# Kernel tuning notes

Measured on AMD Instinct MI355X. Metric: run time of the kernel, lower is better.

Reference implementation:

```python
import jax, jax.numpy as jnp
import numpy as np

N_NODES = 100000
N_EDGES = 1600000
N_GRAPHS = 512


def gcn_conv(x, src, dst, W, b, n_nodes):
    """PyG GCNConv: add self-loops, symmetric norm, linear, scatter-add, bias."""
    h = x @ W.T                                   # [N, out]
    ones = jnp.ones(src.shape[0], dtype=x.dtype)
    deg = jax.ops.segment_sum(ones, dst, num_segments=n_nodes)   # in-degree incl. self-loops
    dinv = jnp.where(deg > 0, jax.lax.rsqrt(deg), 0.0)
    norm = dinv[src] * dinv[dst]                  # [E+N]
    msg = h[src] * norm[:, None]                  # gather + scale
    out = jax.ops.segment_sum(msg, dst, num_segments=n_nodes)
    return out + b


def setup_inputs() -> dict:
    key = jax.random.key(0)
    ks = jax.random.split(key, 8)
    x = jax.random.normal(ks[0], (N_NODES, 2), dtype=jnp.float32)
    edge_index = jax.random.randint(ks[1], (2, N_EDGES), 0, N_NODES, dtype=jnp.int64)
    batch = jnp.sort(jax.random.randint(ks[2], (N_NODES,), 0, N_GRAPHS, dtype=jnp.int64))
    def glorot(k, shape):
        lim = jnp.sqrt(6.0 / (shape[0] + shape[1])).astype(jnp.float32)
        return jax.random.uniform(k, shape, jnp.float32, -lim, lim)
    return {
        "x": x, "edge_index": edge_index, "batch": batch,
        "W1": glorot(ks[3], (32, 2)),  "b1": jnp.zeros(32, jnp.float32),
        "W2": glorot(ks[4], (64, 32)), "b2": jnp.zeros(64, jnp.float32),
        "W3": glorot(ks[5], (32, 64)), "b3": jnp.zeros(32, jnp.float32),
        "Wfc": glorot(ks[6], (1, 32)), "bfc": jnp.zeros(1, jnp.float32),
    }


def reference(x, edge_index, batch, W1, b1, W2, b2, W3, b3, Wfc, bfc):
    n = x.shape[0]
    loop = jnp.arange(n, dtype=edge_index.dtype)
    src = jnp.concatenate([edge_index[0], loop])  # self-loops appended once
    dst = jnp.concatenate([edge_index[1], loop])

    h = jax.nn.relu(gcn_conv(x, src, dst, W1, b1, n))   # dropout = identity (eval)
    h = jax.nn.relu(gcn_conv(h, src, dst, W2, b2, n))
    h = jax.nn.relu(gcn_conv(h, src, dst, W3, b3, n))

    # global_mean_pool over graph ids
    sums = jax.ops.segment_sum(h, batch, num_segments=N_GRAPHS)
    cnts = jax.ops.segment_sum(jnp.ones((n,), h.dtype), batch, num_segments=N_GRAPHS)
    pooled = sums / jnp.maximum(cnts, 1.0)[:, None]     # [G, 32]
    return pooled @ Wfc.T + bfc                         # [G, 1]
```

## Files before the change

kernel.cpp:

```cpp
#include <hip/hip_runtime.h>
#include <hip/hip_fp16.h>


static constexpr int TPB = 256;
static constexpr int NB1 = 256;
static constexpr int NB_SCAN = 256;
static constexpr int P2CAP = 6144;

__global__ void p1_hist_gptr_kernel(const int* __restrict__ dst, int* __restrict__ hist,
                                    int E, int chunk, int shift, int B,
                                    const int* __restrict__ batch, int* __restrict__ gstart,
                                    int n, int G) {
  int b = blockIdx.x, t = threadIdx.x;
  if (b >= NB1) {
    int i = (b - NB1) * TPB + t;
    if (i >= n) return;
    int bb = batch[i];
    int bp = (i == 0) ? -1 : batch[i - 1];
    for (int g = bp + 1; g <= bb; ++g) gstart[g] = i;
    if (i == n - 1)
      for (int g = bb + 1; g <= G; ++g) gstart[g] = n;
    return;
  }
  __shared__ int h[1024];
  for (int i = t; i < B; i += TPB) h[i] = 0;
  __syncthreads();
  int lo = b * chunk, hi = min(lo + chunk, E);
  for (int e = lo + t; e < hi; e += TPB) atomicAdd(&h[dst[e] >> shift], 1);
  __syncthreads();
  for (int i = t; i < B; i += TPB) hist[i * NB1 + b] = h[i];
}

__global__ void scan_partial_kernel(const int* __restrict__ a, int* __restrict__ bsum,
                                    int n, int seg) {
  int b = blockIdx.x, t = threadIdx.x;
  int lo = b * seg, hi = min(lo + seg, n);
  int acc = 0;
  for (int i = lo + t; i < hi; i += TPB) acc += a[i];
  __shared__ int red[TPB];
  red[t] = acc;
  __syncthreads();
  for (int st = TPB / 2; st > 0; st >>= 1) {
    if (t < st) red[t] += red[t + st];
    __syncthreads();
  }
  if (t == 0) bsum[b] = red[0];
}

__global__ void scan_emit_kernel(int* __restrict__ a, const int* __restrict__ bsum,
                                 int n, int seg) {
  int b = blockIdx.x, t = threadIdx.x;
  int lo = b * seg, hi = min(lo + seg, n);
  __shared__ int cs[TPB];
  __shared__ int s_run;
  cs[t] = (t < b) ? bsum[t] : 0;
  __syncthreads();
  for (int st = TPB / 2; st > 0; st >>= 1) {
    if (t < st) cs[t] += cs[t + st];
    __syncthreads();
  }
  if (t == 0) s_run = cs[0];
  __syncthreads();
  for (int base = lo; base < hi; base += TPB) {
    int i = base + t;
    int v = (i < hi) ? a[i] : 0;
    cs[t] = v;
    __syncthreads();
    for (int off = 1; off < TPB; off <<= 1) {
      int u = (t >= off) ? cs[t - off] : 0;
      __syncthreads();
      cs[t] += u;
      __syncthreads();
    }
    if (i < hi) a[i] = s_run + cs[t] - v;
    __syncthreads();
    if (t == 0) s_run += cs[TPB - 1];
    __syncthreads();
  }
}

__global__ void p1_scatter_kernel(const int* __restrict__ src, const int* __restrict__ dst,
                                  const int* __restrict__ hist, unsigned int* __restrict__ epk,
                                  int E, int chunk, int shift, int srcbits, int B) {
  __shared__ int cur[1024];
  int b = blockIdx.x, t = threadIdx.x;
  for (int i = t; i < B; i += TPB) cur[i] = hist[i * NB1 + b];
  __syncthreads();
  int lo = b * chunk, hi = min(lo + chunk, E);
  int span1 = (1 << shift) - 1;
  for (int e = lo + t; e < hi; e += TPB) {
    int d = dst[e];
    int pos = atomicAdd(&cur[d >> shift], 1);
    epk[pos] = ((unsigned int)(d & span1) << srcbits) | (unsigned int)src[e];
  }
}

__global__ __launch_bounds__(TPB) void p2_sort_kernel(
    const unsigned int* __restrict__ epk, const int* __restrict__ hist,
    const float2* __restrict__ x2,
    int* __restrict__ rowptr, float* __restrict__ dinv, float2* __restrict__ u0,
    int* __restrict__ esrc, int N, int E, int shift, int srcbits, int B) {
  int bkt = blockIdx.x, t = threadIdx.x;
  int span = 1 << shift;
  unsigned int smask = (1u << srcbits) - 1u;
  int nb = bkt << shift;
  int bstart = hist[bkt * NB1];
  int bend = (bkt + 1 < B) ? hist[(bkt + 1) * NB1] : E;
  int bsize = bend - bstart;
  __shared__ int cnt[256];
  __shared__ int ex[256];
  __shared__ int ldata[P2CAP];
  __shared__ int lsrc[P2CAP];
  bool stage = (bsize <= P2CAP);
  if (t < span) cnt[t] = 0;
  __syncthreads();
  if (stage) {
    for (int i = t; i < bsize; i += TPB) ldata[i] = (int)epk[bstart + i];
    __syncthreads();
    for (int i = t; i < bsize; i += TPB)
      atomicAdd(&cnt[((unsigned int)ldata[i]) >> srcbits], 1);
  } else {
    for (int e = bstart + t; e < bend; e += TPB) atomicAdd(&cnt[epk[e] >> srcbits], 1);
  }
  __syncthreads();
  int v = (t < span) ? cnt[t] : 0;
  ex[t] = v;
  __syncthreads();
  for (int off = 1; off < 256; off <<= 1) {
    int u = (t >= off) ? ex[t - off] : 0;
    __syncthreads();
    ex[t] += u;
    __syncthreads();
  }
  int excl = ex[t] - v;
  int node = nb + t;
  if (t < span && node < N) {
    rowptr[node] = bstart + excl;
    float dv = rsqrtf((float)v + 1.0f);
    dinv[node] = dv;
    float2 xv = x2[node];
    u0[node] = make_float2(xv.x * dv, xv.y * dv);
  }
  if (bkt == 0 && t == 0) rowptr[N] = E;
  __syncthreads();
  if (t < span) cnt[t] = stage ? excl : bstart + excl;
  __syncthreads();
  if (stage) {
    for (int i = t; i < bsize; i += TPB) {
      unsigned int p = (unsigned int)ldata[i];
      int pos = atomicAdd(&cnt[p >> srcbits], 1);
      lsrc[pos] = (int)(p & smask);
    }
    __syncthreads();
    for (int i = t; i < bsize; i += TPB) esrc[bstart + i] = lsrc[i];
  } else {
    for (int e = bstart + t; e < bend; e += TPB) {
      unsigned int p = epk[e];
      int pos = atomicAdd(&cnt[p >> srcbits], 1);
      esrc[pos] = (int)(p & smask);
    }
  }
}

__global__ void layer1_kernel(const float2* __restrict__ u0, const int* __restrict__ rowptr,
                              const int* __restrict__ esrc, const float* __restrict__ W1,
                              const float* __restrict__ b1, const float* __restrict__ dinv,
                              __half* __restrict__ u1_16, int n) {
  int tid = blockIdx.x * blockDim.x + threadIdx.x;
  int i = tid >> 2, split = tid & 3;
  if (i >= n) return;
  float ax = 0.f, ay = 0.f;
  if (split == 0) {
    float2 s = u0[i];
    ax = s.x; ay = s.y;
  }
  int r0 = rowptr[i], r1 = rowptr[i + 1];
  int e = r0 + split;
  if (e < r1) {
    int snext = esrc[e];
    for (e += 4; e < r1; e += 4) {
      int scur = snext;
      snext = esrc[e];
      float2 v = u0[scur];
      ax += v.x; ay += v.y;
    }
    float2 v = u0[snext];
    ax += v.x; ay += v.y;
  }
  ax += __shfl_xor(ax, 1, 64); ay += __shfl_xor(ay, 1, 64);
  ax += __shfl_xor(ax, 2, 64); ay += __shfl_xor(ay, 2, 64);
  float di = dinv[i];
  int f0 = split * 8;
  union { float4 f4[1]; __half h[8]; } oh;
#pragma unroll
  for (int k = 0; k < 8; ++k) {
    int f = f0 + k;
    float hv = fmaxf(di * (W1[f * 2 + 0] * ax + W1[f * 2 + 1] * ay) + b1[f], 0.f);
    oh.h[k] = __float2half(di * hv);
  }
  *(float4*)&u1_16[(size_t)i * 32 + f0] = oh.f4[0];
}

template <bool EPI>
__global__ void gather32_kernel(const float4* __restrict__ a16,
                                const int* __restrict__ rowptr, const int* __restrict__ esrc,
                                const float* __restrict__ dinv, const float* __restrict__ b,
                                float4* __restrict__ out16, int n) {
  int tid = blockIdx.x * blockDim.x + threadIdx.x;
  int i = tid >> 4;
  int sub = tid & 15;
  int split = sub >> 2, q = sub & 3;
  if (i >= n) return;
  float acc[8] = {0.f, 0.f, 0.f, 0.f, 0.f, 0.f, 0.f, 0.f};
  auto addrow = [&](int s) {
    union { float4 f4; __half2 h2[4]; } u;
    u.f4 = a16[(size_t)s * 4 + q];
    float2 a0 = __half22float2(u.h2[0]);
    float2 a1 = __half22float2(u.h2[1]);
    float2 a2 = __half22float2(u.h2[2]);
    float2 a3 = __half22float2(u.h2[3]);
    acc[0] += a0.x; acc[1] += a0.y; acc[2] += a1.x; acc[3] += a1.y;
    acc[4] += a2.x; acc[5] += a2.y; acc[6] += a3.x; acc[7] += a3.y;
  };
  if (split == 0) addrow(i);
  int r0 = rowptr[i], r1 = rowptr[i + 1];
  int e = r0 + split;
  if (e < r1) {
    int snext = esrc[e];
    for (e += 4; e < r1; e += 4) {
      int scur = snext;
      snext = esrc[e];
      addrow(scur);
    }
    addrow(snext);
  }
#pragma unroll
  for (int k = 0; k < 8; ++k) acc[k] += __shfl_xor(acc[k], 4, 64);
#pragma unroll
  for (int k = 0; k < 8; ++k) acc[k] += __shfl_xor(acc[k], 8, 64);
  if (split != 0) return;
  if (EPI) {
    float di = dinv[i];
    const float4 bv0 = ((const float4*)b)[2 * q];
    const float4 bv1 = ((const float4*)b)[2 * q + 1];
    acc[0] = fmaxf(di * acc[0] + bv0.x, 0.f);
    acc[1] = fmaxf(di * acc[1] + bv0.y, 0.f);
    acc[2] = fmaxf(di * acc[2] + bv0.z, 0.f);
    acc[3] = fmaxf(di * acc[3] + bv0.w, 0.f);
    acc[4] = fmaxf(di * acc[4] + bv1.x, 0.f);
    acc[5] = fmaxf(di * acc[5] + bv1.y, 0.f);
    acc[6] = fmaxf(di * acc[6] + bv1.z, 0.f);
    acc[7] = fmaxf(di * acc[7] + bv1.w, 0.f);
  }
  union { float4 f4; __half2 h2[4]; } o;
  o.h2[0] = __floats2half2_rn(acc[0], acc[1]);
  o.h2[1] = __floats2half2_rn(acc[2], acc[3]);
  o.h2[2] = __floats2half2_rn(acc[4], acc[5]);
  o.h2[3] = __floats2half2_rn(acc[6], acc[7]);
  out16[(size_t)i * 4 + q] = o.f4;
}

__global__ __launch_bounds__(TPB) void t2t3_kernel(
    const float4* __restrict__ U1h, const float* __restrict__ W2, const float* __restrict__ b2,
    const float* __restrict__ W3, const float* __restrict__ dinv,
    __half* __restrict__ g3_16, int n) {
  constexpr int SN = 136;
  __shared__ float U1l[32 * SN];
  __shared__ float h2l[64 * SN];
  __shared__ float W2l[32 * 68];
  __shared__ float W3l[64 * 36];
  __shared__ float dil[128];
  int t = threadIdx.x;
  int base = blockIdx.x * 128;
  for (int idx = t; idx < 2048; idx += TPB) {
    int k = idx >> 5, j = idx & 31;
    W2l[j * 68 + k] = W2[idx];
  }
  for (int idx = t; idx < 2048; idx += TPB) {
    int k = idx >> 6, j = idx & 63;
    W3l[j * 36 + k] = W3[idx];
  }
  if (t < 128) dil[t] = (base + t < n) ? dinv[base + t] : 0.f;
  for (int it = 0; it < 2; ++it) {
    int idx = it * 256 + t;
    int nl = idx >> 2, j0 = (idx & 3) * 8;
    int node = base + nl;
    union { float4 f4; __half2 h2[4]; } u;
    u.f4 = (node < n) ? U1h[(size_t)node * 4 + (idx & 3)]
                      : make_float4(0.f, 0.f, 0.f, 0.f);
#pragma unroll
    for (int k = 0; k < 4; ++k) {
      float2 p = __half22float2(u.h2[k]);
      U1l[(j0 + 2 * k + 0) * SN + nl] = p.x;
      U1l[(j0 + 2 * k + 1) * SN + nl] = p.y;
    }
  }
  __syncthreads();
  {
    int a = t & 15, bb = t >> 4;
    int n0 = a * 8, k0 = bb * 4;
    float acc[4][8];
#pragma unroll
    for (int kk = 0; kk < 4; ++kk)
#pragma unroll
      for (int nn = 0; nn < 8; ++nn) acc[kk][nn] = 0.f;
#pragma unroll 8
    for (int j = 0; j < 32; ++j) {
      float4 ua = *(const float4*)&U1l[j * SN + n0];
      float4 ub = *(const float4*)&U1l[j * SN + n0 + 4];
      float4 w = *(const float4*)&W2l[j * 68 + k0];
      float un[8] = {ua.x, ua.y, ua.z, ua.w, ub.x, ub.y, ub.z, ub.w};
      float wk[4] = {w.x, w.y, w.z, w.w};
#pragma unroll
      for (int kk = 0; kk < 4; ++kk)
#pragma unroll
        for (int nn = 0; nn < 8; ++nn) acc[kk][nn] += un[nn] * wk[kk];
    }
    float4 bv = ((const float4*)b2)[bb];
    float bk[4] = {bv.x, bv.y, bv.z, bv.w};
#pragma unroll
    for (int kk = 0; kk < 4; ++kk) {
      float o[8];
#pragma unroll
      for (int nn = 0; nn < 8; ++nn)
        o[nn] = fmaxf(dil[n0 + nn] * acc[kk][nn] + bk[kk], 0.f);
      *(float4*)&h2l[(k0 + kk) * SN + n0] = make_float4(o[0], o[1], o[2], o[3]);
      *(float4*)&h2l[(k0 + kk) * SN + n0 + 4] = make_float4(o[4], o[5], o[6], o[7]);
    }
  }
  __syncthreads();
  {
    int a = t & 15, bb = t >> 4;
    int n0 = a * 8, k0 = bb * 2;
    float acc[2][8];
#pragma unroll
    for (int kk = 0; kk < 2; ++kk)
#pragma unroll
      for (int nn = 0; nn < 8; ++nn) acc[kk][nn] = 0.f;
#pragma unroll 8
    for (int j = 0; j < 64; ++j) {
      float4 ua = *(const float4*)&h2l[j * SN + n0];
      float4 ub = *(const float4*)&h2l[j * SN + n0 + 4];
      float w0 = W3l[j * 36 + k0];
      float w1 = W3l[j * 36 + k0 + 1];
      float un[8] = {ua.x, ua.y, ua.z, ua.w, ub.x, ub.y, ub.z, ub.w};
#pragma unroll
      for (int nn = 0; nn < 8; ++nn) {
        acc[0][nn] += un[nn] * w0;
        acc[1][nn] += un[nn] * w1;
      }
    }
#pragma unroll
    for (int nn = 0; nn < 8; ++nn) {
      int node = base + n0 + nn;
      if (node < n) {
        float di = dil[n0 + nn];
        __half2 hv = __floats2half2_rn(di * acc[0][nn], di * acc[1][nn]);
        *(__half2*)&g3_16[(size_t)node * 32 + k0] = hv;
      }
    }
  }
}

__global__ void poolfc_kernel(const __half* __restrict__ h3, const int* __restrict__ gstart,
                              const float* __restrict__ Wfc, const float* __restrict__ bfc,
                              float* __restrict__ out) {
  int gi = blockIdx.x;
  int s = gstart[gi], e = gstart[gi + 1];
  int t = threadIdx.x;
  int nl = t >> 5, f = t & 31;
  float acc = 0.f;
  for (int i = s + nl; i < e; i += 8) acc += __half2float(h3[(size_t)i * 32 + f]);
  __shared__ float red[256];
  red[t] = acc;
  __syncthreads();
  for (int st = 128; st >= 32; st >>= 1) {
    if (t < st) red[t] += red[t + st];
    __syncthreads();
  }
  if (t < 32) {
    float cnt = (float)(e - s);
    float v = (red[t] / fmaxf(cnt, 1.f)) * Wfc[t];
    for (int o = 16; o; o >>= 1) v += __shfl_down(v, o, 32);
    if (t == 0) out[gi] = v + bfc[0];
  }
}

extern "C" void kernel_launch(void* const* d_in, const int* in_sizes, int n_in,
                              void* d_out, int out_size, void* d_ws, size_t ws_size,
                              hipStream_t stream) {
  const float* x     = (const float*)d_in[0];
  const int*   ei    = (const int*)d_in[1];
  const int*   batch = (const int*)d_in[2];
  const float* W1    = (const float*)d_in[3];
  const float* b1    = (const float*)d_in[4];
  const float* W2    = (const float*)d_in[5];
  const float* b2    = (const float*)d_in[6];
  const float* W3    = (const float*)d_in[7];
  const float* b3    = (const float*)d_in[8];
  const float* Wfc   = (const float*)d_in[9];
  const float* bfc   = (const float*)d_in[10];
  float* out = (float*)d_out;

  const int N = in_sizes[0] / 2;
  const int E = in_sizes[1] / 2;
  const int G = out_size;
  const int* src = ei;
  const int* dst = ei + E;

  int shift = 8;
  while ((((N + (1 << shift) - 1) >> shift)) > 1024) ++shift;
  const int B = (N + (1 << shift) - 1) >> shift;
  const int srcbits = 32 - shift;
  const int chunkE = (E + NB1 - 1) / NB1;
  const int M = B * NB1;
  const int segM = (M + NB_SCAN - 1) / NB_SCAN;

  char* ws = (char*)d_ws;
  size_t off = 0;
  auto alloc = [&](size_t bytes) -> char* {
    char* p = ws + off;
    off += (bytes + 255) & ~(size_t)255;
    return p;
  };
  float*        dinv   = (float*)alloc((size_t)N * 4);
  int*          rowptr = (int*)alloc((size_t)(N + 1) * 4);
  int*          esrc   = (int*)alloc((size_t)E * 4);
  int*          gstart = (int*)alloc((size_t)(G + 1) * 4);
  int*          hist   = (int*)alloc((size_t)M * 4);
  int*          bsum   = (int*)alloc((size_t)NB_SCAN * 4);
  unsigned int* epk    = (unsigned int*)alloc((size_t)E * 4);
  float2*       u0     = (float2*)alloc((size_t)N * 8);
  __half*       u1_16  = (__half*)alloc((size_t)N * 32 * 2);
  __half*       U1h    = (__half*)alloc((size_t)N * 32 * 2);
  __half*       g3_16  = (__half*)alloc((size_t)N * 32 * 2);
  __half*       hA16   = (__half*)alloc((size_t)N * 32 * 2);

  const int gptrBlocks = (N + TPB - 1) / TPB;
  p1_hist_gptr_kernel<<<NB1 + gptrBlocks, TPB, 0, stream>>>(dst, hist, E, chunkE, shift, B,
                                                            batch, gstart, N, G);
  scan_partial_kernel<<<NB_SCAN, TPB, 0, stream>>>(hist, bsum, M, segM);
  scan_emit_kernel<<<NB_SCAN, TPB, 0, stream>>>(hist, bsum, M, segM);
  p1_scatter_kernel<<<NB1, TPB, 0, stream>>>(src, dst, hist, epk, E, chunkE, shift, srcbits, B);
  p2_sort_kernel<<<B, TPB, 0, stream>>>(epk, hist, (const float2*)x, rowptr, dinv, u0, esrc,
                                        N, E, shift, srcbits, B);

  layer1_kernel<<<((size_t)N * 4 + TPB - 1) / TPB, TPB, 0, stream>>>(
      u0, rowptr, esrc, W1, b1, dinv, u1_16, N);

  gather32_kernel<false><<<((size_t)N * 16 + TPB - 1) / TPB, TPB, 0, stream>>>(
      (const float4*)u1_16, rowptr, esrc, dinv, b2, (float4*)U1h, N);
  t2t3_kernel<<<(N + 127) / 128, TPB, 0, stream>>>(
      (const float4*)U1h, W2, b2, W3, dinv, g3_16, N);

  gather32_kernel<true><<<((size_t)N * 16 + TPB - 1) / TPB, TPB, 0, stream>>>(
      (const float4*)g3_16, rowptr, esrc, dinv, b3, (float4*)hA16, N);

  poolfc_kernel<<<G, 256, 0, stream>>>(hA16, gstart, Wfc, bfc, out);
}
```

Measured before the change: 220.0 us.

## Fuse layer-2 gather with both dense transforms, unroll edge loops by two

```diff
diff --git a/kernel.cpp b/kernel.cpp
--- a/kernel.cpp
+++ b/kernel.cpp
@@ -176,15 +176,16 @@
   }
   int r0 = rowptr[i], r1 = rowptr[i + 1];
   int e = r0 + split;
+  while (e + 4 < r1) {
+    int s0 = esrc[e], s1 = esrc[e + 4];
+    float2 v0 = u0[s0];
+    float2 v1 = u0[s1];
+    ax += v0.x + v1.x;
+    ay += v0.y + v1.y;
+    e += 8;
+  }
   if (e < r1) {
-    int snext = esrc[e];
-    for (e += 4; e < r1; e += 4) {
-      int scur = snext;
-      snext = esrc[e];
-      float2 v = u0[scur];
-      ax += v.x; ay += v.y;
-    }
-    float2 v = u0[snext];
+    float2 v = u0[esrc[e]];
     ax += v.x; ay += v.y;
   }
   ax += __shfl_xor(ax, 1, 64); ay += __shfl_xor(ay, 1, 64);
@@ -201,20 +202,113 @@
   *(float4*)&u1_16[(size_t)i * 32 + f0] = oh.f4[0];
 }
 
-template <bool EPI>
-__global__ void gather32_kernel(const float4* __restrict__ a16,
-                                const int* __restrict__ rowptr, const int* __restrict__ esrc,
-                                const float* __restrict__ dinv, const float* __restrict__ b,
-                                float4* __restrict__ out16, int n) {
+__global__ __launch_bounds__(TPB) void gather_t2t3_kernel(
+    const float4* __restrict__ a16, const int* __restrict__ rowptr,
+    const int* __restrict__ esrc, const float* __restrict__ dinv,
+    const float* __restrict__ W2, const float* __restrict__ b2,
+    const float* __restrict__ W3, __half* __restrict__ g3_16, int n) {
+  __shared__ float U1l[16 * 33];
+  __shared__ float h2l[16 * 68];
+  __shared__ float W2l[32 * 68];
+  __shared__ float W3l[64 * 36];
+  __shared__ float dil[16];
+  int t = threadIdx.x;
+  int base = blockIdx.x * 16;
+  for (int idx = t; idx < 2048; idx += TPB) {
+    int k = idx >> 5, j = idx & 31;
+    W2l[j * 68 + k] = W2[idx];
+  }
+  for (int idx = t; idx < 2048; idx += TPB) {
+    int k = idx >> 6, j = idx & 63;
+    W3l[j * 36 + k] = W3[idx];
+  }
+  if (t < 16) dil[t] = (base + t < n) ? dinv[base + t] : 0.f;
+
+  int i = base + (t >> 4);
+  int sub = t & 15, split = sub >> 2, q = sub & 3;
+  float acc[8] = {0.f, 0.f, 0.f, 0.f, 0.f, 0.f, 0.f, 0.f};
+  if (i < n) {
+    auto addf4 = [&](float4 f) {
+      union { float4 f4; __half2 h2[4]; } u;
+      u.f4 = f;
+      float2 a0 = __half22float2(u.h2[0]);
+      float2 a1 = __half22float2(u.h2[1]);
+      float2 a2 = __half22float2(u.h2[2]);
+      float2 a3 = __half22float2(u.h2[3]);
+      acc[0] += a0.x; acc[1] += a0.y; acc[2] += a1.x; acc[3] += a1.y;
+      acc[4] += a2.x; acc[5] += a2.y; acc[6] += a3.x; acc[7] += a3.y;
+    };
+    if (split == 0) addf4(a16[(size_t)i * 4 + q]);
+    int r0 = rowptr[i], r1 = rowptr[i + 1];
+    int e = r0 + split;
+    while (e + 4 < r1) {
+      int s0 = esrc[e], s1 = esrc[e + 4];
+      float4 f0 = a16[(size_t)s0 * 4 + q];
+      float4 f1 = a16[(size_t)s1 * 4 + q];
+      addf4(f0);
+      addf4(f1);
+      e += 8;
+    }
+    if (e < r1) addf4(a16[(size_t)esrc[e] * 4 + q]);
+#pragma unroll
+    for (int k = 0; k < 8; ++k) acc[k] += __shfl_xor(acc[k], 4, 64);
+#pragma unroll
+    for (int k = 0; k < 8; ++k) acc[k] += __shfl_xor(acc[k], 8, 64);
+    if (split == 0) {
+      int nl = t >> 4;
+#pragma unroll
+      for (int k = 0; k < 8; ++k) U1l[nl * 33 + q * 8 + k] = acc[k];
+    }
+  }
+  __syncthreads();
+
+  {
+    int nl = t >> 4, k0 = (t & 15) * 4;
+    float a0 = 0.f, a1 = 0.f, a2 = 0.f, a3 = 0.f;
+#pragma unroll 8
+    for (int j = 0; j < 32; ++j) {
+      float u = U1l[nl * 33 + j];
+      float4 w = *(const float4*)&W2l[j * 68 + k0];
+      a0 += u * w.x; a1 += u * w.y; a2 += u * w.z; a3 += u * w.w;
+    }
+    float di = dil[nl];
+    float4 bv = ((const float4*)b2)[t & 15];
+    *(float4*)&h2l[nl * 68 + k0] =
+        make_float4(fmaxf(di * a0 + bv.x, 0.f), fmaxf(di * a1 + bv.y, 0.f),
+                    fmaxf(di * a2 + bv.z, 0.f), fmaxf(di * a3 + bv.w, 0.f));
+  }
+  __syncthreads();
+
+  {
+    int nl = t >> 4, k0 = (t & 15) * 2;
+    float a0 = 0.f, a1 = 0.f;
+#pragma unroll 8
+    for (int j = 0; j < 64; ++j) {
+      float u = h2l[nl * 68 + j];
+      a0 += u * W3l[j * 36 + k0];
+      a1 += u * W3l[j * 36 + k0 + 1];
+    }
+    int node = base + nl;
+    if (node < n) {
+      float di = dil[nl];
+      *(__half2*)&g3_16[(size_t)node * 32 + k0] = __floats2half2_rn(di * a0, di * a1);
+    }
+  }
+}
+
+__global__ void gather32epi_kernel(const float4* __restrict__ a16,
+                                   const int* __restrict__ rowptr, const int* __restrict__ esrc,
+                                   const float* __restrict__ dinv, const float* __restrict__ b,
+                                   float4* __restrict__ out16, int n) {
   int tid = blockIdx.x * blockDim.x + threadIdx.x;
   int i = tid >> 4;
   int sub = tid & 15;
   int split = sub >> 2, q = sub & 3;
   if (i >= n) return;
   float acc[8] = {0.f, 0.f, 0.f, 0.f, 0.f, 0.f, 0.f, 0.f};
-  auto addrow = [&](int s) {
+  auto addf4 = [&](float4 f) {
     union { float4 f4; __half2 h2[4]; } u;
-    u.f4 = a16[(size_t)s * 4 + q];
+    u.f4 = f;
     float2 a0 = __half22float2(u.h2[0]);
     float2 a1 = __half22float2(u.h2[1]);
     float2 a2 = __half22float2(u.h2[2]);
@@ -222,36 +316,34 @@
     acc[0] += a0.x; acc[1] += a0.y; acc[2] += a1.x; acc[3] += a1.y;
     acc[4] += a2.x; acc[5] += a2.y; acc[6] += a3.x; acc[7] += a3.y;
   };
-  if (split == 0) addrow(i);
+  if (split == 0) addf4(a16[(size_t)i * 4 + q]);
   int r0 = rowptr[i], r1 = rowptr[i + 1];
   int e = r0 + split;
-  if (e < r1) {
-    int snext = esrc[e];
-    for (e += 4; e < r1; e += 4) {
-      int scur = snext;
-      snext = esrc[e];
-      addrow(scur);
-    }
-    addrow(snext);
-  }
+  while (e + 4 < r1) {
+    int s0 = esrc[e], s1 = esrc[e + 4];
+    float4 f0 = a16[(size_t)s0 * 4 + q];
+    float4 f1 = a16[(size_t)s1 * 4 + q];
+    addf4(f0);
+    addf4(f1);
+    e += 8;
+  }
+  if (e < r1) addf4(a16[(size_t)esrc[e] * 4 + q]);
 #pragma unroll
   for (int k = 0; k < 8; ++k) acc[k] += __shfl_xor(acc[k], 4, 64);
 #pragma unroll
   for (int k = 0; k < 8; ++k) acc[k] += __shfl_xor(acc[k], 8, 64);
   if (split != 0) return;
-  if (EPI) {
-    float di = dinv[i];
-    const float4 bv0 = ((const float4*)b)[2 * q];
-    const float4 bv1 = ((const float4*)b)[2 * q + 1];
-    acc[0] = fmaxf(di * acc[0] + bv0.x, 0.f);
-    acc[1] = fmaxf(di * acc[1] + bv0.y, 0.f);
-    acc[2] = fmaxf(di * acc[2] + bv0.z, 0.f);
-    acc[3] = fmaxf(di * acc[3] + bv0.w, 0.f);
-    acc[4] = fmaxf(di * acc[4] + bv1.x, 0.f);
-    acc[5] = fmaxf(di * acc[5] + bv1.y, 0.f);
-    acc[6] = fmaxf(di * acc[6] + bv1.z, 0.f);
-    acc[7] = fmaxf(di * acc[7] + bv1.w, 0.f);
-  }
+  float di = dinv[i];
+  const float4 bv0 = ((const float4*)b)[2 * q];
+  const float4 bv1 = ((const float4*)b)[2 * q + 1];
+  acc[0] = fmaxf(di * acc[0] + bv0.x, 0.f);
+  acc[1] = fmaxf(di * acc[1] + bv0.y, 0.f);
+  acc[2] = fmaxf(di * acc[2] + bv0.z, 0.f);
+  acc[3] = fmaxf(di * acc[3] + bv0.w, 0.f);
+  acc[4] = fmaxf(di * acc[4] + bv1.x, 0.f);
+  acc[5] = fmaxf(di * acc[5] + bv1.y, 0.f);
+  acc[6] = fmaxf(di * acc[6] + bv1.z, 0.f);
+  acc[7] = fmaxf(di * acc[7] + bv1.w, 0.f);
   union { float4 f4; __half2 h2[4]; } o;
   o.h2[0] = __floats2half2_rn(acc[0], acc[1]);
   o.h2[1] = __floats2half2_rn(acc[2], acc[3]);
@@ -260,128 +352,29 @@
   out16[(size_t)i * 4 + q] = o.f4;
 }
 
-__global__ __launch_bounds__(TPB) void t2t3_kernel(
-    const float4* __restrict__ U1h, const float* __restrict__ W2, const float* __restrict__ b2,
-    const float* __restrict__ W3, const float* __restrict__ dinv,
-    __half* __restrict__ g3_16, int n) {
-  constexpr int SN = 136;
-  __shared__ float U1l[32 * SN];
-  __shared__ float h2l[64 * SN];
-  __shared__ float W2l[32 * 68];
-  __shared__ float W3l[64 * 36];
-  __shared__ float dil[128];
-  int t = threadIdx.x;
-  int base = blockIdx.x * 128;
-  for (int idx = t; idx < 2048; idx += TPB) {
-    int k = idx >> 5, j = idx & 31;
-    W2l[j * 68 + k] = W2[idx];
-  }
-  for (int idx = t; idx < 2048; idx += TPB) {
-    int k = idx >> 6, j = idx & 63;
-    W3l[j * 36 + k] = W3[idx];
-  }
-  if (t < 128) dil[t] = (base + t < n) ? dinv[base + t] : 0.f;
-  for (int it = 0; it < 2; ++it) {
-    int idx = it * 256 + t;
-    int nl = idx >> 2, j0 = (idx & 3) * 8;
-    int node = base + nl;
-    union { float4 f4; __half2 h2[4]; } u;
-    u.f4 = (node < n) ? U1h[(size_t)node * 4 + (idx & 3)]
-                      : make_float4(0.f, 0.f, 0.f, 0.f);
-#pragma unroll
-    for (int k = 0; k < 4; ++k) {
-      float2 p = __half22float2(u.h2[k]);
-      U1l[(j0 + 2 * k + 0) * SN + nl] = p.x;
-      U1l[(j0 + 2 * k + 1) * SN + nl] = p.y;
-    }
-  }
-  __syncthreads();
-  {
-    int a = t & 15, bb = t >> 4;
-    int n0 = a * 8, k0 = bb * 4;
-    float acc[4][8];
-#pragma unroll
-    for (int kk = 0; kk < 4; ++kk)
-#pragma unroll
-      for (int nn = 0; nn < 8; ++nn) acc[kk][nn] = 0.f;
-#pragma unroll 8
-    for (int j = 0; j < 32; ++j) {
-      float4 ua = *(const float4*)&U1l[j * SN + n0];
-      float4 ub = *(const float4*)&U1l[j * SN + n0 + 4];
-      float4 w = *(const float4*)&W2l[j * 68 + k0];
-      float un[8] = {ua.x, ua.y, ua.z, ua.w, ub.x, ub.y, ub.z, ub.w};
-      float wk[4] = {w.x, w.y, w.z, w.w};
-#pragma unroll
-      for (int kk = 0; kk < 4; ++kk)
-#pragma unroll
-        for (int nn = 0; nn < 8; ++nn) acc[kk][nn] += un[nn] * wk[kk];
-    }
-    float4 bv = ((const float4*)b2)[bb];
-    float bk[4] = {bv.x, bv.y, bv.z, bv.w};
-#pragma unroll
-    for (int kk = 0; kk < 4; ++kk) {
-      float o[8];
-#pragma unroll
-      for (int nn = 0; nn < 8; ++nn)
-        o[nn] = fmaxf(dil[n0 + nn] * acc[kk][nn] + bk[kk], 0.f);
-      *(float4*)&h2l[(k0 + kk) * SN + n0] = make_float4(o[0], o[1], o[2], o[3]);
-      *(float4*)&h2l[(k0 + kk) * SN + n0 + 4] = make_float4(o[4], o[5], o[6], o[7]);
-    }
-  }
-  __syncthreads();
-  {
-    int a = t & 15, bb = t >> 4;
-    int n0 = a * 8, k0 = bb * 2;
-    float acc[2][8];
-#pragma unroll
-    for (int kk = 0; kk < 2; ++kk)
-#pragma unroll
-      for (int nn = 0; nn < 8; ++nn) acc[kk][nn] = 0.f;
-#pragma unroll 8
-    for (int j = 0; j < 64; ++j) {
-      float4 ua = *(const float4*)&h2l[j * SN + n0];
-      float4 ub = *(const float4*)&h2l[j * SN + n0 + 4];
-      float w0 = W3l[j * 36 + k0];
-      float w1 = W3l[j * 36 + k0 + 1];
-      float un[8] = {ua.x, ua.y, ua.z, ua.w, ub.x, ub.y, ub.z, ub.w};
-#pragma unroll
-      for (int nn = 0; nn < 8; ++nn) {
-        acc[0][nn] += un[nn] * w0;
-        acc[1][nn] += un[nn] * w1;
-      }
-    }
-#pragma unroll
-    for (int nn = 0; nn < 8; ++nn) {
-      int node = base + n0 + nn;
-      if (node < n) {
-        float di = dil[n0 + nn];
-        __half2 hv = __floats2half2_rn(di * acc[0][nn], di * acc[1][nn]);
-        *(__half2*)&g3_16[(size_t)node * 32 + k0] = hv;
-      }
-    }
-  }
-}
-
-__global__ void poolfc_kernel(const __half* __restrict__ h3, const int* __restrict__ gstart,
+__global__ void poolfc_kernel(const __half2* __restrict__ h3, const int* __restrict__ gstart,
                               const float* __restrict__ Wfc, const float* __restrict__ bfc,
                               float* __restrict__ out) {
   int gi = blockIdx.x;
   int s = gstart[gi], e = gstart[gi + 1];
   int t = threadIdx.x;
-  int nl = t >> 5, f = t & 31;
-  float acc = 0.f;
-  for (int i = s + nl; i < e; i += 8) acc += __half2float(h3[(size_t)i * 32 + f]);
-  __shared__ float red[256];
-  red[t] = acc;
-  __syncthreads();
-  for (int st = 128; st >= 32; st >>= 1) {
-    if (t < st) red[t] += red[t + st];
-    __syncthreads();
-  }
-  if (t < 32) {
-    float cnt = (float)(e - s);
-    float v = (red[t] / fmaxf(cnt, 1.f)) * Wfc[t];
-    for (int o = 16; o; o >>= 1) v += __shfl_down(v, o, 32);
+  int nl = t >> 4, f2 = t & 15;
+  float ax = 0.f, ay = 0.f;
+  for (int i = s + nl; i < e; i += 16) {
+    float2 v = __half22float2(h3[(size_t)i * 16 + f2]);
+    ax += v.x; ay += v.y;
+  }
+  __shared__ float redx[256], redy[256];
+  redx[t] = ax; redy[t] = ay;
+  __syncthreads();
+  for (int st = 128; st >= 16; st >>= 1) {
+    if (t < st) { redx[t] += redx[t + st]; redy[t] += redy[t + st]; }
+    __syncthreads();
+  }
+  if (t < 16) {
+    float cnt = fmaxf((float)(e - s), 1.f);
+    float v = (redx[t] / cnt) * Wfc[2 * t] + (redy[t] / cnt) * Wfc[2 * t + 1];
+    for (int o = 8; o; o >>= 1) v += __shfl_down(v, o, 16);
     if (t == 0) out[gi] = v + bfc[0];
   }
 }
@@ -432,7 +425,6 @@
   unsigned int* epk    = (unsigned int*)alloc((size_t)E * 4);
   float2*       u0     = (float2*)alloc((size_t)N * 8);
   __half*       u1_16  = (__half*)alloc((size_t)N * 32 * 2);
-  __half*       U1h    = (__half*)alloc((size_t)N * 32 * 2);
   __half*       g3_16  = (__half*)alloc((size_t)N * 32 * 2);
   __half*       hA16   = (__half*)alloc((size_t)N * 32 * 2);
 
@@ -448,13 +440,11 @@
   layer1_kernel<<<((size_t)N * 4 + TPB - 1) / TPB, TPB, 0, stream>>>(
       u0, rowptr, esrc, W1, b1, dinv, u1_16, N);
 
-  gather32_kernel<false><<<((size_t)N * 16 + TPB - 1) / TPB, TPB, 0, stream>>>(
-      (const float4*)u1_16, rowptr, esrc, dinv, b2, (float4*)U1h, N);
-  t2t3_kernel<<<(N + 127) / 128, TPB, 0, stream>>>(
-      (const float4*)U1h, W2, b2, W3, dinv, g3_16, N);
-
-  gather32_kernel<true><<<((size_t)N * 16 + TPB - 1) / TPB, TPB, 0, stream>>>(
+  gather_t2t3_kernel<<<((size_t)N * 16 + TPB - 1) / TPB, TPB, 0, stream>>>(
+      (const float4*)u1_16, rowptr, esrc, dinv, W2, b2, W3, g3_16, N);
+
+  gather32epi_kernel<<<((size_t)N * 16 + TPB - 1) / TPB, TPB, 0, stream>>>(
       (const float4*)g3_16, rowptr, esrc, dinv, b3, (float4*)hA16, N);
 
-  poolfc_kernel<<<G, 256, 0, stream>>>(hA16, gstart, Wfc, bfc, out);
-}
+  poolfc_kernel<<<G, 256, 0, stream>>>((const __half2*)hA16, gstart, Wfc, bfc, out);
+}
```

Result: no change. 217.4 us (-1.2%).

## Replace per-node gather with block-level edge-parallel LDS atomic push aggregation

Applied to the files above, without the earlier changes.

```diff
diff --git a/kernel.cpp b/kernel.cpp
--- a/kernel.cpp
+++ b/kernel.cpp
@@ -102,7 +102,6 @@
     int* __restrict__ esrc, int N, int E, int shift, int srcbits, int B) {
   int bkt = blockIdx.x, t = threadIdx.x;
   int span = 1 << shift;
-  unsigned int smask = (1u << srcbits) - 1u;
   int nb = bkt << shift;
   int bstart = hist[bkt * NB1];
   int bend = (bkt + 1 < B) ? hist[(bkt + 1) * NB1] : E;
@@ -147,9 +146,9 @@
   __syncthreads();
   if (stage) {
     for (int i = t; i < bsize; i += TPB) {
-      unsigned int p = (unsigned int)ldata[i];
-      int pos = atomicAdd(&cnt[p >> srcbits], 1);
-      lsrc[pos] = (int)(p & smask);
+      int p = ldata[i];
+      int pos = atomicAdd(&cnt[((unsigned int)p) >> srcbits], 1);
+      lsrc[pos] = p;
     }
     __syncthreads();
     for (int i = t; i < bsize; i += TPB) esrc[bstart + i] = lsrc[i];
@@ -157,7 +156,7 @@
     for (int e = bstart + t; e < bend; e += TPB) {
       unsigned int p = epk[e];
       int pos = atomicAdd(&cnt[p >> srcbits], 1);
-      esrc[pos] = (int)(p & smask);
+      esrc[pos] = (int)p;
     }
   }
 }
@@ -165,10 +164,11 @@
 __global__ void layer1_kernel(const float2* __restrict__ u0, const int* __restrict__ rowptr,
                               const int* __restrict__ esrc, const float* __restrict__ W1,
                               const float* __restrict__ b1, const float* __restrict__ dinv,
-                              __half* __restrict__ u1_16, int n) {
+                              __half* __restrict__ u1_16, int n, int srcbits) {
   int tid = blockIdx.x * blockDim.x + threadIdx.x;
   int i = tid >> 2, split = tid & 3;
   if (i >= n) return;
+  unsigned int smask = (1u << srcbits) - 1u;
   float ax = 0.f, ay = 0.f;
   if (split == 0) {
     float2 s = u0[i];
@@ -176,15 +176,16 @@
   }
   int r0 = rowptr[i], r1 = rowptr[i + 1];
   int e = r0 + split;
+  while (e + 4 < r1) {
+    int s0 = esrc[e] & smask, s1 = esrc[e + 4] & smask;
+    float2 v0 = u0[s0];
+    float2 v1 = u0[s1];
+    ax += v0.x + v1.x;
+    ay += v0.y + v1.y;
+    e += 8;
+  }
   if (e < r1) {
-    int snext = esrc[e];
-    for (e += 4; e < r1; e += 4) {
-      int scur = snext;
-      snext = esrc[e];
-      float2 v = u0[scur];
-      ax += v.x; ay += v.y;
-    }
-    float2 v = u0[snext];
+    float2 v = u0[esrc[e] & smask];
     ax += v.x; ay += v.y;
   }
   ax += __shfl_xor(ax, 1, 64); ay += __shfl_xor(ay, 1, 64);
@@ -202,45 +203,61 @@
 }
 
 template <bool EPI>
-__global__ void gather32_kernel(const float4* __restrict__ a16,
-                                const int* __restrict__ rowptr, const int* __restrict__ esrc,
-                                const float* __restrict__ dinv, const float* __restrict__ b,
-                                float4* __restrict__ out16, int n) {
-  int tid = blockIdx.x * blockDim.x + threadIdx.x;
-  int i = tid >> 4;
-  int sub = tid & 15;
-  int split = sub >> 2, q = sub & 3;
-  if (i >= n) return;
-  float acc[8] = {0.f, 0.f, 0.f, 0.f, 0.f, 0.f, 0.f, 0.f};
-  auto addrow = [&](int s) {
+__global__ __launch_bounds__(TPB) void gpush_kernel(
+    const float4* __restrict__ a16, const int* __restrict__ rowptr,
+    const int* __restrict__ esrc, const float* __restrict__ dinv,
+    const float* __restrict__ b, float4* __restrict__ out16, int n, int srcbits) {
+  __shared__ float accum[64 * 33];
+  int t = threadIdx.x;
+  int base = blockIdx.x * 64;
+  unsigned int smask = (1u << srcbits) - 1u;
+  int nl = t >> 2, q = t & 3;
+  int node = base + nl;
+  {
     union { float4 f4; __half2 h2[4]; } u;
-    u.f4 = a16[(size_t)s * 4 + q];
-    float2 a0 = __half22float2(u.h2[0]);
-    float2 a1 = __half22float2(u.h2[1]);
-    float2 a2 = __half22float2(u.h2[2]);
-    float2 a3 = __half22float2(u.h2[3]);
-    acc[0] += a0.x; acc[1] += a0.y; acc[2] += a1.x; acc[3] += a1.y;
-    acc[4] += a2.x; acc[5] += a2.y; acc[6] += a3.x; acc[7] += a3.y;
-  };
-  if (split == 0) addrow(i);
-  int r0 = rowptr[i], r1 = rowptr[i + 1];
-  int e = r0 + split;
-  if (e < r1) {
-    int snext = esrc[e];
-    for (e += 4; e < r1; e += 4) {
-      int scur = snext;
-      snext = esrc[e];
-      addrow(scur);
-    }
-    addrow(snext);
-  }
-#pragma unroll
-  for (int k = 0; k < 8; ++k) acc[k] += __shfl_xor(acc[k], 4, 64);
-#pragma unroll
-  for (int k = 0; k < 8; ++k) acc[k] += __shfl_xor(acc[k], 8, 64);
-  if (split != 0) return;
+    u.f4 = (node < n) ? a16[(size_t)node * 4 + q] : make_float4(0.f, 0.f, 0.f, 0.f);
+    float* dstp = &accum[nl * 33 + q * 8];
+#pragma unroll
+    for (int k = 0; k < 4; ++k) {
+      float2 p = __half22float2(u.h2[k]);
+      dstp[2 * k + 0] = p.x;
+      dstp[2 * k + 1] = p.y;
+    }
+  }
+  __syncthreads();
+  int e0 = rowptr[base];
+  int e1 = rowptr[min(base + 64, n)];
+  int ne = e1 - e0;
+  int slot = t >> 2;
+  int nIter = (ne + 63) >> 6;
+  int my0 = slot * nIter;
+  for (int it = 0; it < nIter; ++it) {
+    int ei = my0 + it;
+    if (ei < ne) {
+      unsigned int p = (unsigned int)esrc[e0 + ei];
+      int src = (int)(p & smask);
+      int dl = (int)(p >> srcbits) & 63;
+      union { float4 f4; __half2 h2[4]; } u;
+      u.f4 = a16[(size_t)src * 4 + q];
+      float* ap = &accum[dl * 33 + q * 8];
+#pragma unroll
+      for (int k = 0; k < 4; ++k) {
+        float2 v = __half22float2(u.h2[k]);
+        atomicAdd(&ap[2 * k + 0], v.x);
+        atomicAdd(&ap[2 * k + 1], v.y);
+      }
+    }
+  }
+  __syncthreads();
+  if (node >= n) return;
+  float acc[8];
+  {
+    const float* sp = &accum[nl * 33 + q * 8];
+#pragma unroll
+    for (int k = 0; k < 8; ++k) acc[k] = sp[k];
+  }
   if (EPI) {
-    float di = dinv[i];
+    float di = dinv[node];
     const float4 bv0 = ((const float4*)b)[2 * q];
     const float4 bv1 = ((const float4*)b)[2 * q + 1];
     acc[0] = fmaxf(di * acc[0] + bv0.x, 0.f);
@@ -257,7 +274,7 @@
   o.h2[1] = __floats2half2_rn(acc[2], acc[3]);
   o.h2[2] = __floats2half2_rn(acc[4], acc[5]);
   o.h2[3] = __floats2half2_rn(acc[6], acc[7]);
-  out16[(size_t)i * 4 + q] = o.f4;
+  out16[(size_t)node * 4 + q] = o.f4;
 }
 
 __global__ __launch_bounds__(TPB) void t2t3_kernel(
@@ -362,26 +379,29 @@
   }
 }
 
-__global__ void poolfc_kernel(const __half* __restrict__ h3, const int* __restrict__ gstart,
+__global__ void poolfc_kernel(const __half2* __restrict__ h3, const int* __restrict__ gstart,
                               const float* __restrict__ Wfc, const float* __restrict__ bfc,
                               float* __restrict__ out) {
   int gi = blockIdx.x;
   int s = gstart[gi], e = gstart[gi + 1];
   int t = threadIdx.x;
-  int nl = t >> 5, f = t & 31;
-  float acc = 0.f;
-  for (int i = s + nl; i < e; i += 8) acc += __half2float(h3[(size_t)i * 32 + f]);
-  __shared__ float red[256];
-  red[t] = acc;
-  __syncthreads();
-  for (int st = 128; st >= 32; st >>= 1) {
-    if (t < st) red[t] += red[t + st];
-    __syncthreads();
-  }
-  if (t < 32) {
-    float cnt = (float)(e - s);
-    float v = (red[t] / fmaxf(cnt, 1.f)) * Wfc[t];
-    for (int o = 16; o; o >>= 1) v += __shfl_down(v, o, 32);
+  int nl = t >> 4, f2 = t & 15;
+  float ax = 0.f, ay = 0.f;
+  for (int i = s + nl; i < e; i += 16) {
+    float2 v = __half22float2(h3[(size_t)i * 16 + f2]);
+    ax += v.x; ay += v.y;
+  }
+  __shared__ float redx[256], redy[256];
+  redx[t] = ax; redy[t] = ay;
+  __syncthreads();
+  for (int st = 128; st >= 16; st >>= 1) {
+    if (t < st) { redx[t] += redx[t + st]; redy[t] += redy[t + st]; }
+    __syncthreads();
+  }
+  if (t < 16) {
+    float cnt = fmaxf((float)(e - s), 1.f);
+    float v = (redx[t] / cnt) * Wfc[2 * t] + (redy[t] / cnt) * Wfc[2 * t + 1];
+    for (int o = 8; o; o >>= 1) v += __shfl_down(v, o, 16);
     if (t == 0) out[gi] = v + bfc[0];
   }
 }
@@ -446,15 +466,16 @@
                                         N, E, shift, srcbits, B);
 
   layer1_kernel<<<((size_t)N * 4 + TPB - 1) / TPB, TPB, 0, stream>>>(
-      u0, rowptr, esrc, W1, b1, dinv, u1_16, N);
-
-  gather32_kernel<false><<<((size_t)N * 16 + TPB - 1) / TPB, TPB, 0, stream>>>(
-      (const float4*)u1_16, rowptr, esrc, dinv, b2, (float4*)U1h, N);
+      u0, rowptr, esrc, W1, b1, dinv, u1_16, N, srcbits);
+
+  const int gpushBlocks = (N + 63) / 64;
+  gpush_kernel<false><<<gpushBlocks, TPB, 0, stream>>>(
+      (const float4*)u1_16, rowptr, esrc, dinv, b2, (float4*)U1h, N, srcbits);
   t2t3_kernel<<<(N + 127) / 128, TPB, 0, stream>>>(
       (const float4*)U1h, W2, b2, W3, dinv, g3_16, N);
 
-  gather32_kernel<true><<<((size_t)N * 16 + TPB - 1) / TPB, TPB, 0, stream>>>(
-      (const float4*)g3_16, rowptr, esrc, dinv, b3, (float4*)hA16, N);
-
-  poolfc_kernel<<<G, 256, 0, stream>>>(hA16, gstart, Wfc, bfc, out);
-}
+  gpush_kernel<true><<<gpushBlocks, TPB, 0, stream>>>(
+      (const float4*)g3_16, rowptr, esrc, dinv, b3, (float4*)hA16, N, srcbits);
+
+  poolfc_kernel<<<G, 256, 0, stream>>>((const __half2*)hA16, gstart, Wfc, bfc, out);
+}
```

After: 770.6 us. 3.5x slower.

## Fuse mean-pool into last gather via atomic per-graph sums; unroll layer1 loop

Applied to the files above, without the earlier changes.

```diff
diff --git a/kernel.cpp b/kernel.cpp
--- a/kernel.cpp
+++ b/kernel.cpp
@@ -10,10 +10,11 @@
 __global__ void p1_hist_gptr_kernel(const int* __restrict__ dst, int* __restrict__ hist,
                                     int E, int chunk, int shift, int B,
                                     const int* __restrict__ batch, int* __restrict__ gstart,
-                                    int n, int G) {
+                                    float* __restrict__ gsum, int n, int G) {
   int b = blockIdx.x, t = threadIdx.x;
   if (b >= NB1) {
     int i = (b - NB1) * TPB + t;
+    if (i < G * 32) gsum[i] = 0.f;
     if (i >= n) return;
     int bb = batch[i];
     int bp = (i == 0) ? -1 : batch[i - 1];
@@ -176,15 +177,16 @@
   }
   int r0 = rowptr[i], r1 = rowptr[i + 1];
   int e = r0 + split;
+  while (e + 4 < r1) {
+    int s0 = esrc[e], s1 = esrc[e + 4];
+    float2 v0 = u0[s0];
+    float2 v1 = u0[s1];
+    ax += v0.x + v1.x;
+    ay += v0.y + v1.y;
+    e += 8;
+  }
   if (e < r1) {
-    int snext = esrc[e];
-    for (e += 4; e < r1; e += 4) {
-      int scur = snext;
-      snext = esrc[e];
-      float2 v = u0[scur];
-      ax += v.x; ay += v.y;
-    }
-    float2 v = u0[snext];
+    float2 v = u0[esrc[e]];
     ax += v.x; ay += v.y;
   }
   ax += __shfl_xor(ax, 1, 64); ay += __shfl_xor(ay, 1, 64);
@@ -201,10 +203,8 @@
   *(float4*)&u1_16[(size_t)i * 32 + f0] = oh.f4[0];
 }
 
-template <bool EPI>
 __global__ void gather32_kernel(const float4* __restrict__ a16,
                                 const int* __restrict__ rowptr, const int* __restrict__ esrc,
-                                const float* __restrict__ dinv, const float* __restrict__ b,
                                 float4* __restrict__ out16, int n) {
   int tid = blockIdx.x * blockDim.x + threadIdx.x;
   int i = tid >> 4;
@@ -239,25 +239,68 @@
 #pragma unroll
   for (int k = 0; k < 8; ++k) acc[k] += __shfl_xor(acc[k], 8, 64);
   if (split != 0) return;
-  if (EPI) {
-    float di = dinv[i];
-    const float4 bv0 = ((const float4*)b)[2 * q];
-    const float4 bv1 = ((const float4*)b)[2 * q + 1];
-    acc[0] = fmaxf(di * acc[0] + bv0.x, 0.f);
-    acc[1] = fmaxf(di * acc[1] + bv0.y, 0.f);
-    acc[2] = fmaxf(di * acc[2] + bv0.z, 0.f);
-    acc[3] = fmaxf(di * acc[3] + bv0.w, 0.f);
-    acc[4] = fmaxf(di * acc[4] + bv1.x, 0.f);
-    acc[5] = fmaxf(di * acc[5] + bv1.y, 0.f);
-    acc[6] = fmaxf(di * acc[6] + bv1.z, 0.f);
-    acc[7] = fmaxf(di * acc[7] + bv1.w, 0.f);
-  }
   union { float4 f4; __half2 h2[4]; } o;
   o.h2[0] = __floats2half2_rn(acc[0], acc[1]);
   o.h2[1] = __floats2half2_rn(acc[2], acc[3]);
   o.h2[2] = __floats2half2_rn(acc[4], acc[5]);
   o.h2[3] = __floats2half2_rn(acc[6], acc[7]);
   out16[(size_t)i * 4 + q] = o.f4;
+}
+
+__global__ void gather32pool_kernel(const float4* __restrict__ a16,
+                                    const int* __restrict__ rowptr,
+                                    const int* __restrict__ esrc,
+                                    const float* __restrict__ dinv,
+                                    const float* __restrict__ b,
+                                    const int* __restrict__ batch,
+                                    float* __restrict__ gsum, int n) {
+  int tid = blockIdx.x * blockDim.x + threadIdx.x;
+  int i = tid >> 4;
+  int sub = tid & 15;
+  int split = sub >> 2, q = sub & 3;
+  if (i >= n) return;
+  float acc[8] = {0.f, 0.f, 0.f, 0.f, 0.f, 0.f, 0.f, 0.f};
+  auto addrow = [&](int s) {
+    union { float4 f4; __half2 h2[4]; } u;
+    u.f4 = a16[(size_t)s * 4 + q];
+    float2 a0 = __half22float2(u.h2[0]);
+    float2 a1 = __half22float2(u.h2[1]);
+    float2 a2 = __half22float2(u.h2[2]);
+    float2 a3 = __half22float2(u.h2[3]);
+    acc[0] += a0.x; acc[1] += a0.y; acc[2] += a1.x; acc[3] += a1.y;
+    acc[4] += a2.x; acc[5] += a2.y; acc[6] += a3.x; acc[7] += a3.y;
+  };
+  if (split == 0) addrow(i);
+  int r0 = rowptr[i], r1 = rowptr[i + 1];
+  int e = r0 + split;
+  if (e < r1) {
+    int snext = esrc[e];
+    for (e += 4; e < r1; e += 4) {
+      int scur = snext;
+      snext = esrc[e];
+      addrow(scur);
+    }
+    addrow(snext);
+  }
+#pragma unroll
+  for (int k = 0; k < 8; ++k) acc[k] += __shfl_xor(acc[k], 4, 64);
+#pragma unroll
+  for (int k = 0; k < 8; ++k) acc[k] += __shfl_xor(acc[k], 8, 64);
+  if (split != 0) return;
+  float di = dinv[i];
+  const float4 bv0 = ((const float4*)b)[2 * q];
+  const float4 bv1 = ((const float4*)b)[2 * q + 1];
+  acc[0] = fmaxf(di * acc[0] + bv0.x, 0.f);
+  acc[1] = fmaxf(di * acc[1] + bv0.y, 0.f);
+  acc[2] = fmaxf(di * acc[2] + bv0.z, 0.f);
+  acc[3] = fmaxf(di * acc[3] + bv0.w, 0.f);
+  acc[4] = fmaxf(di * acc[4] + bv1.x, 0.f);
+  acc[5] = fmaxf(di * acc[5] + bv1.y, 0.f);
+  acc[6] = fmaxf(di * acc[6] + bv1.z, 0.f);
+  acc[7] = fmaxf(di * acc[7] + bv1.w, 0.f);
+  float* gp = &gsum[(size_t)batch[i] * 32 + q * 8];
+#pragma unroll
+  for (int k = 0; k < 8; ++k) unsafeAtomicAdd(&gp[k], acc[k]);
 }
 
 __global__ __launch_bounds__(TPB) void t2t3_kernel(
@@ -362,28 +405,16 @@
   }
 }
 
-__global__ void poolfc_kernel(const __half* __restrict__ h3, const int* __restrict__ gstart,
-                              const float* __restrict__ Wfc, const float* __restrict__ bfc,
-                              float* __restrict__ out) {
+__global__ void fcfinish_kernel(const float* __restrict__ gsum, const int* __restrict__ gstart,
+                                const float* __restrict__ Wfc, const float* __restrict__ bfc,
+                                float* __restrict__ out) {
   int gi = blockIdx.x;
-  int s = gstart[gi], e = gstart[gi + 1];
   int t = threadIdx.x;
-  int nl = t >> 5, f = t & 31;
-  float acc = 0.f;
-  for (int i = s + nl; i < e; i += 8) acc += __half2float(h3[(size_t)i * 32 + f]);
-  __shared__ float red[256];
-  red[t] = acc;
-  __syncthreads();
-  for (int st = 128; st >= 32; st >>= 1) {
-    if (t < st) red[t] += red[t + st];
-    __syncthreads();
-  }
-  if (t < 32) {
-    float cnt = (float)(e - s);
-    float v = (red[t] / fmaxf(cnt, 1.f)) * Wfc[t];
-    for (int o = 16; o; o >>= 1) v += __shfl_down(v, o, 32);
-    if (t == 0) out[gi] = v + bfc[0];
-  }
+  if (t >= 32) return;
+  float cnt = fmaxf((float)(gstart[gi + 1] - gstart[gi]), 1.f);
+  float v = (gsum[(size_t)gi * 32 + t] / cnt) * Wfc[t];
+  for (int o = 16; o; o >>= 1) v += __shfl_down(v, o, 32);
+  if (t == 0) out[gi] = v + bfc[0];
 }
 
 extern "C" void kernel_launch(void* const* d_in, const int* in_sizes, int n_in,
@@ -434,11 +465,11 @@
   __half*       u1_16  = (__half*)alloc((size_t)N * 32 * 2);
   __half*       U1h    = (__half*)alloc((size_t)N * 32 * 2);
   __half*       g3_16  = (__half*)alloc((size_t)N * 32 * 2);
-  __half*       hA16   = (__half*)alloc((size_t)N * 32 * 2);
+  float*        gsum   = (float*)alloc((size_t)G * 32 * 4);
 
   const int gptrBlocks = (N + TPB - 1) / TPB;
   p1_hist_gptr_kernel<<<NB1 + gptrBlocks, TPB, 0, stream>>>(dst, hist, E, chunkE, shift, B,
-                                                            batch, gstart, N, G);
+                                                            batch, gstart, gsum, N, G);
   scan_partial_kernel<<<NB_SCAN, TPB, 0, stream>>>(hist, bsum, M, segM);
   scan_emit_kernel<<<NB_SCAN, TPB, 0, stream>>>(hist, bsum, M, segM);
   p1_scatter_kernel<<<NB1, TPB, 0, stream>>>(src, dst, hist, epk, E, chunkE, shift, srcbits, B);
@@ -448,13 +479,13 @@
   layer1_kernel<<<((size_t)N * 4 + TPB - 1) / TPB, TPB, 0, stream>>>(
       u0, rowptr, esrc, W1, b1, dinv, u1_16, N);
 
-  gather32_kernel<false><<<((size_t)N * 16 + TPB - 1) / TPB, TPB, 0, stream>>>(
-      (const float4*)u1_16, rowptr, esrc, dinv, b2, (float4*)U1h, N);
+  gather32_kernel<<<((size_t)N * 16 + TPB - 1) / TPB, TPB, 0, stream>>>(
+      (const float4*)u1_16, rowptr, esrc, (float4*)U1h, N);
   t2t3_kernel<<<(N + 127) / 128, TPB, 0, stream>>>(
       (const float4*)U1h, W2, b2, W3, dinv, g3_16, N);
 
-  gather32_kernel<true><<<((size_t)N * 16 + TPB - 1) / TPB, TPB, 0, stream>>>(
-      (const float4*)g3_16, rowptr, esrc, dinv, b3, (float4*)hA16, N);
-
-  poolfc_kernel<<<G, 256, 0, stream>>>(hA16, gstart, Wfc, bfc, out);
-}
+  gather32pool_kernel<<<((size_t)N * 16 + TPB - 1) / TPB, TPB, 0, stream>>>(
+      (const float4*)g3_16, rowptr, esrc, dinv, b3, batch, gsum, N);
+
+  fcfinish_kernel<<<G, 64, 0, stream>>>(gsum, gstart, Wfc, bfc, out);
+}
```

Result: slower. 386.5 us (+75.7%).
